# Optimization experiments

Hardware: AMD Instinct MI355X
Metric: run time of the kernel (lower is better)

Reference implementation:

```python
import jax, jax.numpy as jnp
import numpy as np
from jax import lax

N = 2048
D_ENC = 64      # conv channels
D = 512         # node embedding dim (resnet18 feature dim)
K = 5           # max_num_neighbors
L_LAYERS = 4    # num_layers
ARENA = 32.0    # positions scaled to [0, ARENA)^2
R2 = 2.0        # radius^2 = (sqrt(2))^2


def setup_inputs() -> dict:
    key = jax.random.key(0)
    ks = jax.random.split(key, 9)
    imgs = jax.random.normal(ks[0], (N, 3, 64, 64), dtype=jnp.float32)
    pos = jax.random.uniform(ks[1], (N, 2), dtype=jnp.float32)  # scaled by ARENA inside
    conv_w = jax.random.normal(ks[2], (D_ENC, 3, 7, 7), dtype=jnp.float32) * 0.05
    conv_b = jnp.zeros((D_ENC,), dtype=jnp.float32)
    proj_w = jax.random.normal(ks[3], (D_ENC, D), dtype=jnp.float32) * (1.0 / np.sqrt(D_ENC))
    proj_b = jnp.zeros((D,), dtype=jnp.float32)
    w_self = jax.random.normal(ks[4], (L_LAYERS, D, D), dtype=jnp.float32) * (1.0 / np.sqrt(D))
    w_nbr = jax.random.normal(ks[5], (L_LAYERS, D, D), dtype=jnp.float32) * (1.0 / np.sqrt(D))
    b_gnn = jnp.zeros((L_LAYERS, D), dtype=jnp.float32)
    return {"imgs": imgs, "pos": pos, "conv_w": conv_w, "conv_b": conv_b,
            "proj_w": proj_w, "proj_b": proj_b,
            "w_self": w_self, "w_nbr": w_nbr, "b_gnn": b_gnn}


def _encode(imgs, conv_w, conv_b, proj_w, proj_b):
    # conv 7x7 stride 2 + relu + global avg pool + linear -> [N, D]
    x = lax.conv_general_dilated(imgs, conv_w, window_strides=(2, 2), padding="SAME",
                                 dimension_numbers=("NCHW", "OIHW", "NCHW"))
    x = jax.nn.relu(x + conv_b[None, :, None, None])
    x = x.mean(axis=(2, 3))                      # [N, D_ENC]
    return jax.nn.relu(x @ proj_w + proj_b)      # [N, D]


def _radius_knn(pos):
    # radius graph with radius sqrt(2), no self loops, capped at K neighbors
    p = pos * ARENA                              # [N, 2]
    d2 = jnp.sum((p[:, None, :] - p[None, :, :]) ** 2, axis=-1)  # [N, N]
    invalid = (d2 > R2) | jnp.eye(N, dtype=bool)
    d2m = jnp.where(invalid, jnp.inf, d2)
    neg_vals, idx = lax.top_k(-d2m, K)           # K nearest within radius
    valid = jnp.isfinite(neg_vals)               # [N, K]
    return idx, valid


def reference(imgs, pos, conv_w, conv_b, proj_w, proj_b, w_self, w_nbr, b_gnn):
    h = _encode(imgs, conv_w, conv_b, proj_w, proj_b)   # [N, D]
    idx, valid = _radius_knn(pos)                        # [N, K], [N, K]
    vmask = valid.astype(h.dtype)                        # [N, K]
    denom = jnp.maximum(vmask.sum(axis=1, keepdims=True), 1.0)  # [N, 1]
    for l in range(L_LAYERS):
        nbr = h[idx] * vmask[:, :, None]                 # [N, K, D] gather
        agg = nbr.sum(axis=1) / denom                    # mean over valid neighbors
        h = jax.nn.relu(h @ w_self[l] + agg @ w_nbr[l] + b_gnn[l])
    return h
```

## Files before the change

kernel.cpp:

```cpp
#include <hip/hip_runtime.h>


#define NNODES 2048

typedef __attribute__((ext_vector_type(8))) _Float16 half8;
typedef __attribute__((ext_vector_type(16))) float f32x16;

__global__ __launch_bounds__(256) void prep_wfrag_kernel(
    const float* __restrict__ w, ushort* __restrict__ wfrag) {
  int i = blockIdx.x * 256 + threadIdx.x;
  if (i >= 12288) return;
  int j = i & 7;
  int l = (i >> 3) & 63;
  int q = i >> 9;
  int kb = q % 12, ct = q / 12;
  int g = 2 * kb + (l >> 5);
  int c = 32 * ct + (l & 31);
  float val = 0.f;
  if (g < 21 && j < 7) val = w[c * 147 + g * 7 + j];
  wfrag[i] = __builtin_bit_cast(ushort, (_Float16)val);
}

__global__ __launch_bounds__(256) void prep_wT_kernel(
    const float* __restrict__ wsrc_s, const float* __restrict__ wsrc_n,
    ushort* __restrict__ wT) {
  __shared__ float s[64][65];
  int bid = blockIdx.x;
  int m = bid >> 6, kt = (bid >> 3) & 7, nt = bid & 7;
  const float* in = (m < 4) ? (wsrc_s + m * 262144) : (wsrc_n + (m - 4) * 262144);
  ushort* out = wT + m * 262144;
  int t = threadIdx.x;
  int k0 = kt << 6, n0 = nt << 6;
#pragma unroll
  for (int rep = 0; rep < 4; ++rep) {
    int row = (rep << 4) + (t >> 4);
    int c4 = (t & 15) << 2;
    float4 v = *(const float4*)&in[(k0 + row) * 512 + n0 + c4];
    s[row][c4] = v.x; s[row][c4 + 1] = v.y; s[row][c4 + 2] = v.z; s[row][c4 + 3] = v.w;
  }
  __syncthreads();
#pragma unroll
  for (int rep = 0; rep < 4; ++rep) {
    int n = (rep << 4) + (t >> 4);
    int k4 = (t & 15) << 2;
    ushort4 o;
    o.x = __builtin_bit_cast(ushort, (_Float16)s[k4 + 0][n]);
    o.y = __builtin_bit_cast(ushort, (_Float16)s[k4 + 1][n]);
    o.z = __builtin_bit_cast(ushort, (_Float16)s[k4 + 2][n]);
    o.w = __builtin_bit_cast(ushort, (_Float16)s[k4 + 3][n]);
    *(ushort4*)&out[(n0 + n) * 512 + k0 + k4] = o;
  }
}

__device__ inline uint pack2h(float x, float y) {
  ushort a = __builtin_bit_cast(ushort, (_Float16)x);
  ushort b = __builtin_bit_cast(ushort, (_Float16)y);
  return (uint)a | ((uint)b << 16);
}

__global__ __launch_bounds__(256) void conv_pool_kernel(
    const float* __restrict__ imgs, const ushort* __restrict__ wfrag,
    const float* __restrict__ cb, float* __restrict__ enc) {
  __shared__ ushort s_img[14904];
  __shared__ float s_pool[64];
  const int n = blockIdx.x;
  const int tid = threadIdx.x;
  const int lane = tid & 63;
  const int w = tid >> 6;
  const int hi = lane >> 5;
  const int lo = lane & 31;

  half8 bf[24];
  const half8* wf = (const half8*)wfrag;
#pragma unroll
  for (int q = 0; q < 24; ++q) bf[q] = wf[q * 64 + lane];

  int4 z = {0, 0, 0, 0};
  for (int i = tid; i < 1863; i += 256) ((int4*)s_img)[i] = z;
  if (tid < 64) s_pool[tid] = 0.f;
  __syncthreads();

  const float4* src = (const float4*)(imgs + (size_t)n * 12288);
  for (int i = tid; i < 3072; i += 256) {
    float4 v = src[i];
    int e = i << 2;
    int c = e >> 12;
    int rem = e & 4095;
    int y = rem >> 6, x = rem & 63;
    int d = (c * 69 + y + 2) * 72 + x + 2;
    ((uint*)s_img)[d >> 1] = pack2h(v.x, v.y);
    ((uint*)s_img)[(d >> 1) + 1] = pack2h(v.z, v.w);
  }

  int boff[12];
#pragma unroll
  for (int kb = 0; kb < 12; ++kb) {
    int g = 2 * kb + hi;
    if (g > 20) g = 20;
    int ic = g / 7, ky = g - ic * 7;
    boff[kb] = (ic * 69 + ky) * 144 + 4 * lo;
  }
  const float bias0 = cb[lo];
  const float bias1 = cb[32 + lo];
  float pool0 = 0.f, pool1 = 0.f;
  __syncthreads();

  const char* sb = (const char*)s_img;
  for (int t = 0; t < 8; ++t) {
    int pt = (w << 3) + t;
    int tadd = pt * 288;
    f32x16 acc0 = {}, acc1 = {};
#pragma unroll
    for (int kb = 0; kb < 12; ++kb) {
      const char* p = sb + boff[kb] + tadd;
      union { half8 v; uint u[4]; } af;
      af.u[0] = *(const uint*)(p);
      af.u[1] = *(const uint*)(p + 4);
      af.u[2] = *(const uint*)(p + 8);
      af.u[3] = *(const uint*)(p + 12);
      acc0 = __builtin_amdgcn_mfma_f32_32x32x16_f16(af.v, bf[kb], acc0, 0, 0, 0);
      acc1 = __builtin_amdgcn_mfma_f32_32x32x16_f16(af.v, bf[12 + kb], acc1, 0, 0, 0);
    }
    float s0 = 0.f, s1 = 0.f;
#pragma unroll
    for (int r = 0; r < 16; ++r) {
      s0 += fmaxf(acc0[r] + bias0, 0.f);
      s1 += fmaxf(acc1[r] + bias1, 0.f);
    }
    pool0 += s0;
    pool1 += s1;
  }
  pool0 += __shfl_xor(pool0, 32);
  pool1 += __shfl_xor(pool1, 32);
  if (lane < 32) {
    atomicAdd(&s_pool[lo], pool0);
    atomicAdd(&s_pool[32 + lo], pool1);
  }
  __syncthreads();
  if (tid < 64) enc[n * 64 + tid] = s_pool[tid] * (1.f / 1024.f);
}

__global__ __launch_bounds__(256) void proj_kernel(
    const float* __restrict__ enc, const float* __restrict__ pw,
    const float* __restrict__ pb, ushort* __restrict__ h16) {
  int c = ((blockIdx.x & 1) << 8) | threadIdx.x;
  int r0 = (blockIdx.x >> 1) << 3;
  float bias = pb[c];
  float acc[8];
#pragma unroll
  for (int r = 0; r < 8; ++r) acc[r] = bias;
#pragma unroll 4
  for (int k = 0; k < 64; ++k) {
    float w = pw[k * 512 + c];
#pragma unroll
    for (int r = 0; r < 8; ++r) acc[r] = fmaf(enc[(r0 + r) * 64 + k], w, acc[r]);
  }
#pragma unroll
  for (int r = 0; r < 8; ++r)
    h16[(r0 + r) * 512 + c] = __builtin_bit_cast(ushort, (_Float16)fmaxf(acc[r], 0.f));
}

__global__ __launch_bounds__(256) void knn_kernel(
    const float* __restrict__ pos, int* __restrict__ nbr, float* __restrict__ den) {
  __shared__ float s_d2[NNODES];
  __shared__ int s_idx[NNODES];
  __shared__ int s_cnt;
  const int i = blockIdx.x;
  const int tid = threadIdx.x;
  if (tid == 0) s_cnt = 0;
  __syncthreads();
  const float px = pos[2 * i] * 32.f, py = pos[2 * i + 1] * 32.f;
#pragma unroll
  for (int r = 0; r < 8; ++r) {
    int j = tid + (r << 8);
    float2 q = ((const float2*)pos)[j];
    float dx = q.x * 32.f - px, dy = q.y * 32.f - py;
    float d2 = dx * dx + dy * dy;
    if (d2 <= 2.0f && j != i) {
      int slot = atomicAdd(&s_cnt, 1);
      s_d2[slot] = d2;
      s_idx[slot] = j;
    }
  }
  __syncthreads();
  if (tid < 64) {
    const int lane = tid;
    const int cnt = s_cnt;
    int nf = 0;
#pragma unroll
    for (int k = 0; k < 5; ++k) {
      float best = 1e30f;
      int bslot = 0x7fffffff;
      for (int e = lane; e < cnt; e += 64) {
        float d = s_d2[e];
        if (d < best) { best = d; bslot = e; }
      }
#pragma unroll
      for (int off = 1; off < 64; off <<= 1) {
        float od = __shfl_xor(best, off);
        int os = __shfl_xor(bslot, off);
        if (od < best || (od == best && os < bslot)) { best = od; bslot = os; }
      }
      bool got = (best < 1e30f);
      if (lane == 0) nbr[i * 5 + k] = got ? s_idx[bslot] : -1;
      if (got) { s_d2[bslot] = 1e30f; ++nf; }
    }
    if (lane == 0) den[i] = (float)(nf > 0 ? nf : 1);
  }
}

__global__ __launch_bounds__(256) void agg_kernel(
    const ushort* __restrict__ h16, const int* __restrict__ nbr,
    const float* __restrict__ den, ushort* __restrict__ agg16) {
  int i = blockIdx.x >> 1;
  int d = ((blockIdx.x & 1) << 8) + threadIdx.x;
  const _Float16* hp = (const _Float16*)h16;
  float s = 0.f;
#pragma unroll
  for (int k = 0; k < 5; ++k) {
    int j = nbr[i * 5 + k];
    if (j >= 0) s += (float)hp[j * 512 + d];
  }
  agg16[i * 512 + d] = __builtin_bit_cast(ushort, (_Float16)(s / den[i]));
}

__global__ __launch_bounds__(256) void gnn_gemm_kernel(
    const ushort* __restrict__ A0, const ushort* __restrict__ A1,
    const ushort* __restrict__ B0, const ushort* __restrict__ B1,
    const float* __restrict__ bias, ushort* __restrict__ hout,
    float* __restrict__ fout, int final_layer) {
  __shared__ ushort s_lds[2][8192];
  const int tid = threadIdx.x;
  const int lane = tid & 63;
  const int hi = lane >> 5, lo = lane & 31;
  const int wu = __builtin_amdgcn_readfirstlane(tid >> 6);
  const int wr = wu >> 1, wc = wu & 1;
  const int bm = blockIdx.x >> 3, bn = blockIdx.x & 7;
  const int r0 = bm << 6, c0 = bn << 6;

  auto STAGE = [&](int buf, int it) {
    const ushort* A = (it & 8) ? A1 : A0;
    const ushort* B = (it & 8) ? B1 : B0;
    int k0 = (it & 7) << 6;
    const ushort* a0 = A + (r0 + lane) * 512 + k0 + 8 * wu;
    const ushort* b0 = B + (c0 + lane) * 512 + k0 + 8 * wu;
    ushort* lb = &s_lds[buf][wu << 9];
    __builtin_amdgcn_global_load_lds(
        (const __attribute__((address_space(1))) void*)(a0),
        (__attribute__((address_space(3))) void*)(lb), 16, 0, 0);
    __builtin_amdgcn_global_load_lds(
        (const __attribute__((address_space(1))) void*)(a0 + 32),
        (__attribute__((address_space(3))) void*)(lb + 2048), 16, 0, 0);
    __builtin_amdgcn_global_load_lds(
        (const __attribute__((address_space(1))) void*)(b0),
        (__attribute__((address_space(3))) void*)(lb + 4096), 16, 0, 0);
    __builtin_amdgcn_global_load_lds(
        (const __attribute__((address_space(1))) void*)(b0 + 32),
        (__attribute__((address_space(3))) void*)(lb + 6144), 16, 0, 0);
  };

  f32x16 acc = {};
  STAGE(0, 0);
  __syncthreads();
  int cur = 0;
  for (int it = 0; it < 16; ++it) {
    if (it < 15) STAGE(cur ^ 1, it + 1);
    const half8* pA = (const half8*)&s_lds[cur][0];
    const half8* pB = (const half8*)&s_lds[cur][4096];
#pragma unroll
    for (int ks = 0; ks < 4; ++ks) {
      half8 af = pA[(2 * ks + hi) * 64 + 32 * wr + lo];
      half8 bfr = pB[(2 * ks + hi) * 64 + 32 * wc + lo];
      acc = __builtin_amdgcn_mfma_f32_32x32x16_f16(af, bfr, acc, 0, 0, 0);
    }
    __syncthreads();
    cur ^= 1;
  }

  const int col = c0 + 32 * wc + lo;
  const float b = bias[col];
#pragma unroll
  for (int r = 0; r < 16; ++r) {
    int row = r0 + 32 * wr + (r & 3) + ((r >> 2) << 3) + (hi << 2);
    float v = fmaxf(acc[r] + b, 0.f);
    if (final_layer) fout[row * 512 + col] = v;
    else hout[row * 512 + col] = __builtin_bit_cast(ushort, (_Float16)v);
  }
}

extern "C" void kernel_launch(void* const* d_in, const int* in_sizes, int n_in,
                              void* d_out, int out_size, void* d_ws, size_t ws_size,
                              hipStream_t stream) {
  const float* imgs   = (const float*)d_in[0];
  const float* pos    = (const float*)d_in[1];
  const float* conv_w = (const float*)d_in[2];
  const float* conv_b = (const float*)d_in[3];
  const float* proj_w = (const float*)d_in[4];
  const float* proj_b = (const float*)d_in[5];
  const float* w_self = (const float*)d_in[6];
  const float* w_nbr  = (const float*)d_in[7];
  const float* b_gnn  = (const float*)d_in[8];

  char* ws = (char*)d_ws;
  ushort* wfrag = (ushort*)(ws);
  float*  enc   = (float*) (ws + 32768);
  ushort* h16a  = (ushort*)(ws + 557056);
  ushort* h16b  = (ushort*)(ws + 2654208);
  ushort* agg16 = (ushort*)(ws + 4751360);
  ushort* wT16  = (ushort*)(ws + 6848512);
  int*    nbr   = (int*)   (ws + 11042816);
  float*  den   = (float*) (ws + 11083776);

  prep_wfrag_kernel<<<48, 256, 0, stream>>>(conv_w, wfrag);
  prep_wT_kernel<<<512, 256, 0, stream>>>(w_self, w_nbr, wT16);
  knn_kernel<<<NNODES, 256, 0, stream>>>(pos, nbr, den);
  conv_pool_kernel<<<NNODES, 256, 0, stream>>>(imgs, wfrag, conv_b, enc);
  proj_kernel<<<512, 256, 0, stream>>>(enc, proj_w, proj_b, h16a);

  for (int l = 0; l < 4; ++l) {
    ushort* hin  = (l & 1) ? h16b : h16a;
    ushort* hnew = (l & 1) ? h16a : h16b;
    agg_kernel<<<4096, 256, 0, stream>>>(hin, nbr, den, agg16);
    gnn_gemm_kernel<<<256, 256, 0, stream>>>(
        hin, agg16, wT16 + l * 262144, wT16 + (4 + l) * 262144,
        b_gnn + l * 512, hnew, (float*)d_out, (l == 3) ? 1 : 0);
  }
}
```

Before: 167.4 us.

## Widen conv MFMA tiles, split GNN GEMM accumulators, use reciprocal denominators

```diff
diff --git a/kernel.cpp b/kernel.cpp
--- a/kernel.cpp
+++ b/kernel.cpp
@@ -92,13 +92,13 @@
     ((uint*)s_img)[(d >> 1) + 1] = pack2h(v.z, v.w);
   }
 
-  int boff[12];
+  int aoff[12];
 #pragma unroll
   for (int kb = 0; kb < 12; ++kb) {
     int g = 2 * kb + hi;
     if (g > 20) g = 20;
     int ic = g / 7, ky = g - ic * 7;
-    boff[kb] = (ic * 69 + ky) * 144 + 4 * lo;
+    aoff[kb] = (ic * 69 + ky) * 144 + 4 * lo + w * 2304;
   }
   const float bias0 = cb[lo];
   const float bias1 = cb[32 + lo];
@@ -106,26 +106,30 @@
   __syncthreads();
 
   const char* sb = (const char*)s_img;
-  for (int t = 0; t < 8; ++t) {
-    int pt = (w << 3) + t;
-    int tadd = pt * 288;
-    f32x16 acc0 = {}, acc1 = {};
+  for (int tp = 0; tp < 4; ++tp) {
+    f32x16 a0 = {}, a1 = {}, a2 = {}, a3 = {};
 #pragma unroll
     for (int kb = 0; kb < 12; ++kb) {
-      const char* p = sb + boff[kb] + tadd;
-      union { half8 v; uint u[4]; } af;
-      af.u[0] = *(const uint*)(p);
-      af.u[1] = *(const uint*)(p + 4);
-      af.u[2] = *(const uint*)(p + 8);
-      af.u[3] = *(const uint*)(p + 12);
-      acc0 = __builtin_amdgcn_mfma_f32_32x32x16_f16(af.v, bf[kb], acc0, 0, 0, 0);
-      acc1 = __builtin_amdgcn_mfma_f32_32x32x16_f16(af.v, bf[12 + kb], acc1, 0, 0, 0);
+      const char* p = sb + aoff[kb] + tp * 576;
+      union { half8 v; uint u[4]; } f0, f1;
+      f0.u[0] = *(const uint*)(p);
+      f0.u[1] = *(const uint*)(p + 4);
+      f0.u[2] = *(const uint*)(p + 8);
+      f0.u[3] = *(const uint*)(p + 12);
+      f1.u[0] = *(const uint*)(p + 288);
+      f1.u[1] = *(const uint*)(p + 292);
+      f1.u[2] = *(const uint*)(p + 296);
+      f1.u[3] = *(const uint*)(p + 300);
+      a0 = __builtin_amdgcn_mfma_f32_32x32x16_f16(f0.v, bf[kb],      a0, 0, 0, 0);
+      a1 = __builtin_amdgcn_mfma_f32_32x32x16_f16(f0.v, bf[12 + kb], a1, 0, 0, 0);
+      a2 = __builtin_amdgcn_mfma_f32_32x32x16_f16(f1.v, bf[kb],      a2, 0, 0, 0);
+      a3 = __builtin_amdgcn_mfma_f32_32x32x16_f16(f1.v, bf[12 + kb], a3, 0, 0, 0);
     }
     float s0 = 0.f, s1 = 0.f;
 #pragma unroll
     for (int r = 0; r < 16; ++r) {
-      s0 += fmaxf(acc0[r] + bias0, 0.f);
-      s1 += fmaxf(acc1[r] + bias1, 0.f);
+      s0 += fmaxf(a0[r] + bias0, 0.f) + fmaxf(a2[r] + bias0, 0.f);
+      s1 += fmaxf(a1[r] + bias1, 0.f) + fmaxf(a3[r] + bias1, 0.f);
     }
     pool0 += s0;
     pool1 += s1;
@@ -205,7 +209,7 @@
       if (lane == 0) nbr[i * 5 + k] = got ? s_idx[bslot] : -1;
       if (got) { s_d2[bslot] = 1e30f; ++nf; }
     }
-    if (lane == 0) den[i] = (float)(nf > 0 ? nf : 1);
+    if (lane == 0) den[i] = 1.f / (float)(nf > 0 ? nf : 1);
   }
 }
 
@@ -221,15 +225,15 @@
     int j = nbr[i * 5 + k];
     if (j >= 0) s += (float)hp[j * 512 + d];
   }
-  agg16[i * 512 + d] = __builtin_bit_cast(ushort, (_Float16)(s / den[i]));
+  agg16[i * 512 + d] = __builtin_bit_cast(ushort, (_Float16)(s * den[i]));
 }
 
 __global__ __launch_bounds__(256) void gnn_gemm_kernel(
-    const ushort* __restrict__ A0, const ushort* __restrict__ A1,
-    const ushort* __restrict__ B0, const ushort* __restrict__ B1,
+    const ushort* __restrict__ hA, const ushort* __restrict__ agg,
+    const ushort* __restrict__ Ws, const ushort* __restrict__ Wn,
     const float* __restrict__ bias, ushort* __restrict__ hout,
     float* __restrict__ fout, int final_layer) {
-  __shared__ ushort s_lds[2][8192];
+  __shared__ ushort s_lds[2][16384];
   const int tid = threadIdx.x;
   const int lane = tid & 63;
   const int hi = lane >> 5, lo = lane & 31;
@@ -239,39 +243,41 @@
   const int r0 = bm << 6, c0 = bn << 6;
 
   auto STAGE = [&](int buf, int it) {
-    const ushort* A = (it & 8) ? A1 : A0;
-    const ushort* B = (it & 8) ? B1 : B0;
-    int k0 = (it & 7) << 6;
-    const ushort* a0 = A + (r0 + lane) * 512 + k0 + 8 * wu;
-    const ushort* b0 = B + (c0 + lane) * 512 + k0 + 8 * wu;
+    int k0 = it << 6;
+    const ushort* ph = hA  + (r0 + lane) * 512 + k0 + 8 * wu;
+    const ushort* pg = agg + (r0 + lane) * 512 + k0 + 8 * wu;
+    const ushort* ps = Ws  + (c0 + lane) * 512 + k0 + 8 * wu;
+    const ushort* pn = Wn  + (c0 + lane) * 512 + k0 + 8 * wu;
     ushort* lb = &s_lds[buf][wu << 9];
-    __builtin_amdgcn_global_load_lds(
-        (const __attribute__((address_space(1))) void*)(a0),
-        (__attribute__((address_space(3))) void*)(lb), 16, 0, 0);
-    __builtin_amdgcn_global_load_lds(
-        (const __attribute__((address_space(1))) void*)(a0 + 32),
-        (__attribute__((address_space(3))) void*)(lb + 2048), 16, 0, 0);
-    __builtin_amdgcn_global_load_lds(
-        (const __attribute__((address_space(1))) void*)(b0),
-        (__attribute__((address_space(3))) void*)(lb + 4096), 16, 0, 0);
-    __builtin_amdgcn_global_load_lds(
-        (const __attribute__((address_space(1))) void*)(b0 + 32),
-        (__attribute__((address_space(3))) void*)(lb + 6144), 16, 0, 0);
+#define GLDS(SRC, DST) __builtin_amdgcn_global_load_lds( \
+      (const __attribute__((address_space(1))) void*)(SRC), \
+      (__attribute__((address_space(3))) void*)(DST), 16, 0, 0)
+    GLDS(ph, lb);            GLDS(ph + 32, lb + 2048);
+    GLDS(pg, lb + 4096);     GLDS(pg + 32, lb + 6144);
+    GLDS(ps, lb + 8192);     GLDS(ps + 32, lb + 10240);
+    GLDS(pn, lb + 12288);    GLDS(pn + 32, lb + 14336);
+#undef GLDS
   };
 
-  f32x16 acc = {};
+  f32x16 accS = {}, accN = {};
   STAGE(0, 0);
   __syncthreads();
   int cur = 0;
-  for (int it = 0; it < 16; ++it) {
-    if (it < 15) STAGE(cur ^ 1, it + 1);
-    const half8* pA = (const half8*)&s_lds[cur][0];
-    const half8* pB = (const half8*)&s_lds[cur][4096];
+  for (int it = 0; it < 8; ++it) {
+    if (it < 7) STAGE(cur ^ 1, it + 1);
+    const half8* pAh = (const half8*)&s_lds[cur][0];
+    const half8* pAg = (const half8*)&s_lds[cur][4096];
+    const half8* pBs = (const half8*)&s_lds[cur][8192];
+    const half8* pBn = (const half8*)&s_lds[cur][12288];
 #pragma unroll
     for (int ks = 0; ks < 4; ++ks) {
-      half8 af = pA[(2 * ks + hi) * 64 + 32 * wr + lo];
-      half8 bfr = pB[(2 * ks + hi) * 64 + 32 * wc + lo];
-      acc = __builtin_amdgcn_mfma_f32_32x32x16_f16(af, bfr, acc, 0, 0, 0);
+      int gi = (2 * ks + hi) * 64;
+      half8 ah = pAh[gi + 32 * wr + lo];
+      half8 bs = pBs[gi + 32 * wc + lo];
+      accS = __builtin_amdgcn_mfma_f32_32x32x16_f16(ah, bs, accS, 0, 0, 0);
+      half8 ag = pAg[gi + 32 * wr + lo];
+      half8 bn2 = pBn[gi + 32 * wc + lo];
+      accN = __builtin_amdgcn_mfma_f32_32x32x16_f16(ag, bn2, accN, 0, 0, 0);
     }
     __syncthreads();
     cur ^= 1;
@@ -282,7 +288,7 @@
 #pragma unroll
   for (int r = 0; r < 16; ++r) {
     int row = r0 + 32 * wr + (r & 3) + ((r >> 2) << 3) + (hi << 2);
-    float v = fmaxf(acc[r] + b, 0.f);
+    float v = fmaxf(accS[r] + accN[r] + b, 0.f);
     if (final_layer) fout[row * 512 + col] = v;
     else hout[row * 512 + col] = __builtin_bit_cast(ushort, (_Float16)v);
   }
```

Result: faster. 160.3 us (-4.2%).
